# Kernel optimization log

Measured on AMD Instinct MI355X. Metric: run time of the kernel, lower is better.

Reference implementation:

```python
import jax, jax.numpy as jnp
import numpy as np

B = 1_048_576
NUM_USERS = 6041
NUM_MOVIES = 3953
EMB_DIM = 32
NUM_GENRES = 18
HIDDEN = [64, 32, 16]
WIDE_DIM = NUM_USERS + NUM_MOVIES + 3 + NUM_GENRES  # gender, age, occupation scalars
DEEP_IN = 2 * EMB_DIM + 3 + NUM_GENRES              # = 85


def setup_inputs() -> dict:
    key = jax.random.key(0)
    ks = jax.random.split(key, 20)
    inp = {
        "user_ids": jax.random.randint(ks[0], (B,), 0, NUM_USERS),
        "movie_ids": jax.random.randint(ks[1], (B,), 0, NUM_MOVIES),
        "gender": jax.random.uniform(ks[2], (B,), dtype=jnp.float32),
        "age": jax.random.uniform(ks[3], (B,), dtype=jnp.float32),
        "occupation": jax.random.uniform(ks[4], (B,), dtype=jnp.float32),
        "genres": jax.random.uniform(ks[5], (B, NUM_GENRES), dtype=jnp.float32),
        # wide linear (out_features=1): weight vector + scalar bias
        "wide_W": jax.random.normal(ks[6], (WIDE_DIM,), dtype=jnp.float32) * 0.01,
        "wide_b": jnp.zeros((), dtype=jnp.float32),
        # embedding tables
        "user_table": jax.random.normal(ks[7], (NUM_USERS, EMB_DIM), dtype=jnp.float32) * 0.05,
        "movie_table": jax.random.normal(ks[8], (NUM_MOVIES, EMB_DIM), dtype=jnp.float32) * 0.05,
        # deep MLP params (stored as [in, out])
        "W1": jax.random.normal(ks[9], (DEEP_IN, HIDDEN[0]), dtype=jnp.float32) * 0.05,
        "b1": jnp.zeros((HIDDEN[0],), dtype=jnp.float32),
        "W2": jax.random.normal(ks[10], (HIDDEN[0], HIDDEN[1]), dtype=jnp.float32) * 0.05,
        "b2": jnp.zeros((HIDDEN[1],), dtype=jnp.float32),
        "W3": jax.random.normal(ks[11], (HIDDEN[1], HIDDEN[2]), dtype=jnp.float32) * 0.05,
        "b3": jnp.zeros((HIDDEN[2],), dtype=jnp.float32),
        "W4": jax.random.normal(ks[12], (HIDDEN[2], 1), dtype=jnp.float32) * 0.05,
        "b4": jnp.zeros((1,), dtype=jnp.float32),
    }
    return inp


def reference(user_ids, movie_ids, gender, age, occupation, genres,
              wide_W, wide_b, user_table, movie_table,
              W1, b1, W2, b2, W3, b3, W4, b4):
    nu = user_table.shape[0]
    nm = movie_table.shape[0]
    # dense (non-one-hot) part of the wide input: [B, 3 + num_genres]
    rest = jnp.concatenate(
        [gender[:, None], age[:, None], occupation[:, None], genres], axis=1)
    # one_hot @ W  ==  gather of the corresponding weight entries (same math,
    # without materializing the [B, nu+nm+21] one-hot matrix)
    w_user = wide_W[:nu]
    w_movie = wide_W[nu:nu + nm]
    w_rest = wide_W[nu + nm:]
    wide_out = w_user[user_ids] + w_movie[movie_ids] + rest @ w_rest + wide_b  # [B]

    # deep path (dropout is identity at inference)
    u_emb = user_table[user_ids]    # [B, 32]
    m_emb = movie_table[movie_ids]  # [B, 32]
    h = jnp.concatenate([u_emb, m_emb, rest], axis=1)  # [B, 85]
    h = jax.nn.relu(h @ W1 + b1)
    h = jax.nn.relu(h @ W2 + b2)
    h = jax.nn.relu(h @ W3 + b3)
    deep_out = (h @ W4 + b4)[:, 0]  # [B]

    return jax.nn.sigmoid(wide_out + deep_out)  # [B]
```

## Files before the change

### kernel.cpp

```cpp
#include <hip/hip_runtime.h>

#define NUSERS  6041
#define NMOVIES 3953
#define EMB     32
#define NGEN    18
#define H1N     64
#define H2N     32
#define H3N     16

typedef __bf16 bf16_t;
typedef bf16_t bf16x8 __attribute__((ext_vector_type(8)));
typedef bf16_t bf16x4 __attribute__((ext_vector_type(4)));
typedef float  f32x4  __attribute__((ext_vector_type(4)));
typedef float  f32x8  __attribute__((ext_vector_type(8)));

__device__ __forceinline__ f32x4 mfma16(bf16x8 a, bf16x8 b, f32x4 c) {
    return __builtin_amdgcn_mfma_f32_16x16x32_bf16(a, b, c, 0, 0, 0);
}
__device__ __forceinline__ bf16x8 cvt8(f32x8 v) {
    bf16x8 o;
    #pragma unroll
    for (int i = 0; i < 8; ++i) o[i] = (bf16_t)v[i];
    return o;
}

#define L1STRIDE 68
#define L2STRIDE 36
#define RSTRIDE  28
#define RBUFSZ   (16 * RSTRIDE)

#define TAB_U4   (NUSERS * EMB / 4)
#define TAB_M4   (NMOVIES * EMB / 4)
#define TAB4TOT  (TAB_U4 + TAB_M4)
#define TABBLOCKS ((TAB4TOT + 255) / 256)

#define WPACK_HALF 9216
#define WPACK_BYTES 18432

__global__ __launch_bounds__(256)
void prep_pack(const float* __restrict__ user_table,
               const float* __restrict__ movie_table,
               const float* __restrict__ W1,
               const float* __restrict__ b1,
               const float* __restrict__ W2,
               const float* __restrict__ W3,
               const float* __restrict__ wide_W,
               bf16_t* __restrict__ utab,
               bf16_t* __restrict__ mtab,
               bf16_t* __restrict__ wpack)
{
    const int t = threadIdx.x;
    const int b = blockIdx.x;

    if (b < TABBLOCKS) {
        const int u = b * 256 + t;
        if (u < TAB4TOT) {
            if (u < TAB_U4) {
                float4 v = *(const float4*)(user_table + (size_t)u * 4);
                bf16x4 o; o[0]=(bf16_t)v.x; o[1]=(bf16_t)v.y; o[2]=(bf16_t)v.z; o[3]=(bf16_t)v.w;
                *(bf16x4*)(utab + (size_t)u * 4) = o;
            } else {
                const int w = u - TAB_U4;
                float4 v = *(const float4*)(movie_table + (size_t)w * 4);
                bf16x4 o; o[0]=(bf16_t)v.x; o[1]=(bf16_t)v.y; o[2]=(bf16_t)v.z; o[3]=(bf16_t)v.w;
                *(bf16x4*)(mtab + (size_t)w * 4) = o;
            }
        }
        return;
    }

    const int l  = t & 63;
    const int f0 = t >> 6;
    const int m  = l & 15;
    const int q  = l >> 4;
    const float* wr = wide_W + NUSERS + NMOVIES;

    #pragma unroll
    for (int p = 0; p < 5; ++p) {
        const int f = f0 + p * 4;
        if (f >= 18) break;
        bf16x8 frag;
        #pragma unroll
        for (int j = 0; j < 8; ++j) {
            float v = 0.0f;
            if (f < 12) {
                const int kt = f >> 2, nt = f & 3;
                if (kt < 2) {
                    v = W1[(kt * 32 + q * 8 + j) * H1N + nt * 16 + m];
                } else if (q < 3) {
                    if (j < 6)       v = W1[(67 + 6 * q + j) * H1N + nt * 16 + m];
                    else if (q == 0) v = W1[(64 + (j - 6)) * H1N + nt * 16 + m];
                    else if (q == 1) v = (j == 6) ? W1[66 * H1N + nt * 16 + m]
                                                 : b1[nt * 16 + m];
                }
            } else if (f == 12) {
                if (m == 0) {
                    if (q < 3 && j < 6)        v = wr[3 + 6 * q + j];
                    else if (q == 0)           v = wr[j - 6];
                    else if (q == 1 && j == 6) v = wr[2];
                    else if (q == 2 && j == 6) v = 1.0f;
                }
            } else if (f < 17) {
                const int kt = (f - 13) >> 1, nt = (f - 13) & 1;
                const int u = (2 * kt + (j >> 2)) * 16 + q * 4 + (j & 3);
                v = W2[u * H2N + nt * 16 + m];
            } else {
                const int u = (j >> 2) * 16 + q * 4 + (j & 3);
                v = W3[u * H3N + m];
            }
            frag[j] = (bf16_t)v;
        }
        *(bf16x8*)(wpack + ((size_t)f * 64 + l) * 8) = frag;
    }
}

__global__ __launch_bounds__(256, 2)
void wd_fwd_main2(const int*   __restrict__ user_ids,
                  const int*   __restrict__ movie_ids,
                  const float* __restrict__ gender,
                  const float* __restrict__ age,
                  const float* __restrict__ occupation,
                  const float* __restrict__ genres,
                  const float* __restrict__ wide_W,
                  const float* __restrict__ wide_b,
                  const float* __restrict__ b2,
                  const float* __restrict__ b3,
                  const float* __restrict__ W4,
                  const float* __restrict__ b4,
                  const bf16_t* __restrict__ utab,
                  const bf16_t* __restrict__ mtab,
                  const bf16_t* __restrict__ wpack,
                  float*       __restrict__ out,
                  int n)
{
    const int lane = threadIdx.x & 63;
    const int m    = lane & 15;
    const int quad = lane >> 4;

    const bf16x8* wp = (const bf16x8*)wpack;
    bf16x8 B1f[3][4];
    #pragma unroll
    for (int kt = 0; kt < 3; ++kt)
        #pragma unroll
        for (int nt = 0; nt < 4; ++nt)
            B1f[kt][nt] = wp[(kt * 4 + nt) * 64 + lane];
    const bf16x8 Bwf = wp[12 * 64 + lane];
    bf16x8 B2f[2][2];
    #pragma unroll
    for (int kt = 0; kt < 2; ++kt)
        #pragma unroll
        for (int nt = 0; nt < 2; ++nt)
            B2f[kt][nt] = wp[(13 + kt * 2 + nt) * 64 + lane];
    const bf16x8 B3f = wp[17 * 64 + lane];

    f32x4 bias2[2], bias3, w4f;
    bias2[0] = *(const f32x4*)(b2 + quad * 4);
    bias2[1] = *(const f32x4*)(b2 + 16 + quad * 4);
    bias3    = *(const f32x4*)(b3 + quad * 4);
    w4f      = *(const f32x4*)(W4 + quad * 4);
    const float b4v = b4[0];
    const float wb0 = wide_b[0];

    const int nst   = (n + 31) >> 5;
    const int gwave = (blockIdx.x * blockDim.x + threadIdx.x) >> 6;
    const int nw    = (gridDim.x * blockDim.x) >> 6;
    int niter = 0;
    if (gwave < nst) niter = (nst - gwave + nw - 1) / nw;
    if (niter == 0) return;

    int st_c = gwave;
    int st_n = st_c + nw; if (st_n >= nst) st_n = st_c;

#define GATHER(row_, uid_, mid_, A0_, A1_, A2_) {                              \
    A0_ = *(const bf16x8*)(utab + (size_t)(uid_) * EMB + quad * 8);            \
    A1_ = *(const bf16x8*)(mtab + (size_t)(mid_) * EMB + quad * 8);            \
    float2 g01 = {0.f,0.f}, g23 = {0.f,0.f}, g45 = {0.f,0.f};                  \
    float s6 = 0.f, s7 = 0.f;                                                  \
    if (quad < 3) {                                                            \
        const float* gp_ = genres + (size_t)(row_) * NGEN + quad * 6;          \
        g01 = *(const float2*)gp_;                                             \
        g23 = *(const float2*)(gp_ + 2);                                       \
        g45 = *(const float2*)(gp_ + 4);                                       \
    }                                                                          \
    if (quad == 0)      { s6 = gender[row_]; s7 = age[row_]; }                 \
    else if (quad == 1) { s6 = occupation[row_]; s7 = 1.0f; }                  \
    else if (quad == 2) { s6 = wide_W[uid_] + wide_W[NUSERS + (mid_)] + wb0; } \
    A2_[0] = (bf16_t)g01.x; A2_[1] = (bf16_t)g01.y;                            \
    A2_[2] = (bf16_t)g23.x; A2_[3] = (bf16_t)g23.y;                            \
    A2_[4] = (bf16_t)g45.x; A2_[5] = (bf16_t)g45.y;                            \
    A2_[6] = (bf16_t)s6;    A2_[7] = (bf16_t)s7; }

    int ra = st_c * 32 + m;      if (ra >= n) ra = n - 1;
    int rb = st_c * 32 + 16 + m; if (rb >= n) rb = n - 1;
    int uidA = user_ids[ra], midA = movie_ids[ra];
    int uidB = user_ids[rb], midB = movie_ids[rb];
    bf16x8 A0a, A1a, A2a, A0b, A1b, A2b;
    GATHER(ra, uidA, midA, A0a, A1a, A2a);
    GATHER(rb, uidB, midB, A0b, A1b, A2b);
    int ran = st_n * 32 + m;      if (ran >= n) ran = n - 1;
    int rbn = st_n * 32 + 16 + m; if (rbn >= n) rbn = n - 1;
    int uidAn = user_ids[ran], midAn = movie_ids[ran];
    int uidBn = user_ids[rbn], midBn = movie_ids[rbn];

    for (int i = 0; i < niter; ++i) {
        const bool more = (i + 1 < niter);
        bf16x8 A0an = A0a, A1an = A1a, A2an = A2a;
        bf16x8 A0bn = A0b, A1bn = A1b, A2bn = A2b;
        int uidA2 = uidAn, midA2 = midAn, uidB2 = uidBn, midB2 = midBn;
        int st_n2 = st_n;
        if (more) {
            int ran_ = st_n * 32 + m;      if (ran_ >= n) ran_ = n - 1;
            int rbn_ = st_n * 32 + 16 + m; if (rbn_ >= n) rbn_ = n - 1;
            GATHER(ran_, uidAn, midAn, A0an, A1an, A2an);
            GATHER(rbn_, uidBn, midBn, A0bn, A1bn, A2bn);
            st_n2 = st_n + nw; if (st_n2 >= nst) st_n2 = st_n;
            int ra2 = st_n2 * 32 + m;      if (ra2 >= n) ra2 = n - 1;
            int rb2 = st_n2 * 32 + 16 + m; if (rb2 >= n) rb2 = n - 1;
            uidA2 = user_ids[ra2]; midA2 = movie_ids[ra2];
            uidB2 = user_ids[rb2]; midB2 = movie_ids[rb2];
        }

        const f32x4 z4 = {0.f, 0.f, 0.f, 0.f};
        f32x4 accwA = mfma16(Bwf, A2a, z4);
        f32x4 accwB = mfma16(Bwf, A2b, z4);

        f32x4 aA[4], aB[4];
        #pragma unroll
        for (int nt = 0; nt < 4; ++nt) {
            aA[nt] = mfma16(B1f[2][nt], A2a, z4);
            aB[nt] = mfma16(B1f[2][nt], A2b, z4);
        }
        #pragma unroll
        for (int nt = 0; nt < 4; ++nt) {
            aA[nt] = mfma16(B1f[1][nt], A1a, aA[nt]);
            aB[nt] = mfma16(B1f[1][nt], A1b, aB[nt]);
        }
        #pragma unroll
        for (int nt = 0; nt < 4; ++nt) {
            aA[nt] = mfma16(B1f[0][nt], A0a, aA[nt]);
            aB[nt] = mfma16(B1f[0][nt], A0b, aB[nt]);
        }

        bf16x8 L2a[2], L2b[2];
        #pragma unroll
        for (int kt = 0; kt < 2; ++kt)
            #pragma unroll
            for (int r = 0; r < 4; ++r) {
                L2a[kt][r]     = (bf16_t)fmaxf(aA[2 * kt][r],     0.f);
                L2a[kt][4 + r] = (bf16_t)fmaxf(aA[2 * kt + 1][r], 0.f);
                L2b[kt][r]     = (bf16_t)fmaxf(aB[2 * kt][r],     0.f);
                L2b[kt][4 + r] = (bf16_t)fmaxf(aB[2 * kt + 1][r], 0.f);
            }

        f32x4 c2A[2], c2B[2];
        #pragma unroll
        for (int nt = 0; nt < 2; ++nt) {
            c2A[nt] = mfma16(B2f[1][nt], L2a[1], mfma16(B2f[0][nt], L2a[0], bias2[nt]));
            c2B[nt] = mfma16(B2f[1][nt], L2b[1], mfma16(B2f[0][nt], L2b[0], bias2[nt]));
        }

        bf16x8 L3a, L3b;
        #pragma unroll
        for (int r = 0; r < 4; ++r) {
            L3a[r]     = (bf16_t)fmaxf(c2A[0][r], 0.f);
            L3a[4 + r] = (bf16_t)fmaxf(c2A[1][r], 0.f);
            L3b[r]     = (bf16_t)fmaxf(c2B[0][r], 0.f);
            L3b[4 + r] = (bf16_t)fmaxf(c2B[1][r], 0.f);
        }

        f32x4 c3A = mfma16(B3f, L3a, bias3);
        f32x4 c3B = mfma16(B3f, L3b, bias3);

        float pA = fmaxf(c3A[0], 0.f) * w4f[0] + fmaxf(c3A[1], 0.f) * w4f[1]
                 + fmaxf(c3A[2], 0.f) * w4f[2] + fmaxf(c3A[3], 0.f) * w4f[3];
        float pB = fmaxf(c3B[0], 0.f) * w4f[0] + fmaxf(c3B[1], 0.f) * w4f[1]
                 + fmaxf(c3B[2], 0.f) * w4f[2] + fmaxf(c3B[3], 0.f) * w4f[3];
        pA += __shfl_xor(pA, 16, 64);  pA += __shfl_xor(pA, 32, 64);
        pB += __shfl_xor(pB, 16, 64);  pB += __shfl_xor(pB, 32, 64);

        if (lane < 16) {
            const int base = st_c << 5;
            const int oa = base + lane, ob = base + 16 + lane;
            const float zA = pA + accwA[0] + b4v;
            const float zB = pB + accwB[0] + b4v;
            if (oa < n) out[oa] = 1.0f / (1.0f + __expf(-zA));
            if (ob < n) out[ob] = 1.0f / (1.0f + __expf(-zB));
        }

        if (more) {
            A0a = A0an; A1a = A1an; A2a = A2an;
            A0b = A0bn; A1b = A1bn; A2b = A2bn;
            uidAn = uidA2; midAn = midA2; uidBn = uidB2; midBn = midB2;
            st_c = st_n; st_n = st_n2;
        }
    }
#undef GATHER
}

struct Pref {
    float4 u0, u1, m0, m1;
    float  wu, wm;
};

__global__ __launch_bounds__(256)
void wd_fwd_pipe(const int*   __restrict__ user_ids,
                 const int*   __restrict__ movie_ids,
                 const float* __restrict__ gender,
                 const float* __restrict__ age,
                 const float* __restrict__ occupation,
                 const float* __restrict__ genres,
                 const float* __restrict__ wide_W,
                 const float* __restrict__ wide_b,
                 const float* __restrict__ user_table,
                 const float* __restrict__ movie_table,
                 const float* __restrict__ W1,
                 const float* __restrict__ b1,
                 const float* __restrict__ W2,
                 const float* __restrict__ b2,
                 const float* __restrict__ W3,
                 const float* __restrict__ b3,
                 const float* __restrict__ W4,
                 const float* __restrict__ b4,
                 float*       __restrict__ out,
                 int n)
{
    const int lane = threadIdx.x & 63;
    const int wib  = threadIdx.x >> 6;
    const int m    = lane & 15;
    const int quad = lane >> 4;

    __shared__ float lds_rest[4][2 * RBUFSZ];
    __shared__ float lds1[4][16 * L1STRIDE];
    __shared__ float lds2[4][16 * L2STRIDE];
    float* __restrict__ rbase = lds_rest[wib];
    float* __restrict__ L1p   = lds1[wib];
    float* __restrict__ L2p   = lds2[wib];

    for (int k = lane; k < 2 * RBUFSZ; k += 64) rbase[k] = 0.0f;

    bf16x8 B1f[3][4];
    #pragma unroll
    for (int kt = 0; kt < 3; ++kt)
        #pragma unroll
        for (int nt = 0; nt < 4; ++nt) {
            bf16x8 f;
            #pragma unroll
            for (int j = 0; j < 8; ++j) {
                const int k  = kt * 32 + quad * 8 + j;
                const float v = (k < 85) ? W1[k * H1N + nt * 16 + m] : 0.0f;
                f[j] = (bf16_t)v;
            }
            B1f[kt][nt] = f;
        }
    bf16x8 Bwf;
    {
        const float* wr = wide_W + NUSERS + NMOVIES;
        #pragma unroll
        for (int j = 0; j < 8; ++j) {
            const int k = 64 + quad * 8 + j;
            float v = 0.0f;
            if (m == 0) { if (k < 85) v = wr[k - 64]; else if (k == 85) v = 1.0f; }
            Bwf[j] = (bf16_t)v;
        }
    }
    bf16x8 B2f[2][2];
    #pragma unroll
    for (int kt = 0; kt < 2; ++kt)
        #pragma unroll
        for (int nt = 0; nt < 2; ++nt) {
            bf16x8 f;
            #pragma unroll
            for (int j = 0; j < 8; ++j)
                f[j] = (bf16_t)W2[(kt * 32 + quad * 8 + j) * H2N + nt * 16 + m];
            B2f[kt][nt] = f;
        }
    bf16x8 B3f;
    #pragma unroll
    for (int j = 0; j < 8; ++j) B3f[j] = (bf16_t)W3[(quad * 8 + j) * H3N + m];

    float bias1[4], bias2[2];
    #pragma unroll
    for (int nt = 0; nt < 4; ++nt) bias1[nt] = b1[nt * 16 + m];
    #pragma unroll
    for (int nt = 0; nt < 2; ++nt) bias2[nt] = b2[nt * 16 + m];
    const float bias3 = b3[m];
    const float w4v   = W4[m];
    const float b4v   = b4[0];
    const float wb0   = wide_b[0];

    const int ntiles = (n + 15) >> 4;
    const int gwave  = blockIdx.x * 4 + wib;
    const int nwaves = gridDim.x * 4;
    int niter = 0;
    if (gwave < ntiles) niter = (ntiles - gwave + nwaves - 1) / nwaves;
    const long gmax = (long)n * NGEN - 1;

#define LOAD_IDS(tt, U, M) { int rr = (tt) * 16 + m; rr = rr < n ? rr : n - 1; \
                             U = user_ids[rr]; M = movie_ids[rr]; }
#define LOAD_GENRES(tt, G, SC) { \
    const long gb = (long)(tt) * (16 * NGEN); \
    _Pragma("unroll") \
    for (int r = 0; r < 4; ++r) { long idx = gb + lane + r * 64; \
        idx = idx < gmax ? idx : gmax; G[r] = genres[idx]; } \
    { long idx = gb + lane + 256; idx = idx < gmax ? idx : gmax; \
      G[4] = (lane < 32) ? genres[idx] : 0.0f; } \
    { int rr = (tt) * 16 + m; rr = rr < n ? rr : n - 1; \
      const float* sp = (quad == 0) ? gender : (quad == 1) ? age : occupation; \
      SC = (quad < 3) ? sp[rr] : 0.0f; } }
#define WRITE_RBUF(B, G, SC) { \
    float* rb_ = rbase + (B) * RBUFSZ; \
    _Pragma("unroll") \
    for (int r = 0; r < 4; ++r) { int gi = lane + r * 64; int rw = gi / NGEN; \
        int cl = gi - rw * NGEN; rb_[rw * RSTRIDE + 3 + cl] = G[r]; } \
    if (lane < 32) { int gi = lane + 256; int rw = gi / NGEN; int cl = gi - rw * NGEN; \
        rb_[rw * RSTRIDE + 3 + cl] = G[4]; } \
    if (quad < 3) rb_[m * RSTRIDE + quad] = SC; }
#define ISSUE_GATHER(UID, MID, P) { \
    const float4* up_ = (const float4*)(user_table + (size_t)(UID) * EMB + quad * 8); \
    P.u0 = up_[0]; P.u1 = up_[1]; \
    const float4* mp_ = (const float4*)(movie_table + (size_t)(MID) * EMB + quad * 8); \
    P.m0 = mp_[0]; P.m1 = mp_[1]; \
    P.wu = wide_W[UID]; P.wm = wide_W[NUSERS + (MID)]; }

    if (niter > 0) {
        int t_c = gwave;
        int t_n = t_c + nwaves; if (t_n >= ntiles) t_n = t_c;

        int uid_c, mid_c, uid_n, mid_n, uid_n2, mid_n2;
        float gg_c[5], sc_c, gg_n[5], sc_n;
        Pref P_c, P_n;

        LOAD_IDS(t_c, uid_c, mid_c);
        LOAD_GENRES(t_c, gg_c, sc_c);
        ISSUE_GATHER(uid_c, mid_c, P_c);
        LOAD_IDS(t_n, uid_n, mid_n);
        WRITE_RBUF(0, gg_c, sc_c);
        uid_n2 = uid_n; mid_n2 = mid_n;
        int buf = 0;

        for (int i = 0; i < niter; ++i) {
            const float* rb = rbase + buf * RBUFSZ;
            const float4* sA = (const float4*)(rb + m * RSTRIDE + quad * 8);
            float4 a2a = sA[0], a2b = sA[1];

            const bool more = (i + 1 < niter);
            int t_n2 = t_n;
            if (more) {
                LOAD_GENRES(t_n, gg_n, sc_n);
                ISSUE_GATHER(uid_n, mid_n, P_n);
                t_n2 = t_n + nwaves; if (t_n2 >= ntiles) t_n2 = t_n;
                LOAD_IDS(t_n2, uid_n2, mid_n2);
            }

            const int base = t_c << 4;
            f32x8 vf;
            vf[0]=P_c.u0.x; vf[1]=P_c.u0.y; vf[2]=P_c.u0.z; vf[3]=P_c.u0.w;
            vf[4]=P_c.u1.x; vf[5]=P_c.u1.y; vf[6]=P_c.u1.z; vf[7]=P_c.u1.w;
            bf16x8 A0 = cvt8(vf);
            vf[0]=P_c.m0.x; vf[1]=P_c.m0.y; vf[2]=P_c.m0.z; vf[3]=P_c.m0.w;
            vf[4]=P_c.m1.x; vf[5]=P_c.m1.y; vf[6]=P_c.m1.z; vf[7]=P_c.m1.w;
            bf16x8 A1 = cvt8(vf);
            vf[0]=a2a.x; vf[1]=a2a.y; vf[2]=a2a.z; vf[3]=a2a.w;
            vf[4]=a2b.x; vf[5]=a2b.y; vf[6]=a2b.z; vf[7]=a2b.w;
            if (quad == 2) vf[5] = P_c.wu + P_c.wm + wb0;
            bf16x8 A2 = cvt8(vf);

            f32x4 accw = mfma16(A2, Bwf, (f32x4){0.f, 0.f, 0.f, 0.f});

            f32x4 acc[4];
            #pragma unroll
            for (int nt = 0; nt < 4; ++nt) {
                f32x4 c = {bias1[nt], bias1[nt], bias1[nt], bias1[nt]};
                c = mfma16(A0, B1f[0][nt], c);
                c = mfma16(A1, B1f[1][nt], c);
                c = mfma16(A2, B1f[2][nt], c);
                acc[nt] = c;
            }
            #pragma unroll
            for (int nt = 0; nt < 4; ++nt)
                #pragma unroll
                for (int r = 0; r < 4; ++r)
                    L1p[(quad * 4 + r) * L1STRIDE + nt * 16 + m] = fmaxf(acc[nt][r], 0.0f);

            bf16x8 AL2[2];
            #pragma unroll
            for (int kt = 0; kt < 2; ++kt) {
                const float4* s = (const float4*)(L1p + m * L1STRIDE + kt * 32 + quad * 8);
                float4 a = s[0], b = s[1];
                f32x8 t8; t8[0]=a.x; t8[1]=a.y; t8[2]=a.z; t8[3]=a.w;
                t8[4]=b.x; t8[5]=b.y; t8[6]=b.z; t8[7]=b.w;
                AL2[kt] = cvt8(t8);
            }

            f32x4 acc2[2];
            #pragma unroll
            for (int nt = 0; nt < 2; ++nt) {
                f32x4 c = {bias2[nt], bias2[nt], bias2[nt], bias2[nt]};
                c = mfma16(AL2[0], B2f[0][nt], c);
                c = mfma16(AL2[1], B2f[1][nt], c);
                acc2[nt] = c;
            }
            #pragma unroll
            for (int nt = 0; nt < 2; ++nt)
                #pragma unroll
                for (int r = 0; r < 4; ++r)
                    L2p[(quad * 4 + r) * L2STRIDE + nt * 16 + m] = fmaxf(acc2[nt][r], 0.0f);

            bf16x8 AL3;
            {
                const float4* s = (const float4*)(L2p + m * L2STRIDE + quad * 8);
                float4 a = s[0], b = s[1];
                f32x8 t8; t8[0]=a.x; t8[1]=a.y; t8[2]=a.z; t8[3]=a.w;
                t8[4]=b.x; t8[5]=b.y; t8[6]=b.z; t8[7]=b.w;
                AL3 = cvt8(t8);
            }

            f32x4 acc3 = mfma16(AL3, B3f, (f32x4){bias3, bias3, bias3, bias3});

            float t0 = fmaxf(acc3[0], 0.0f) * w4v + accw[0];
            float t1 = fmaxf(acc3[1], 0.0f) * w4v + accw[1];
            float t2 = fmaxf(acc3[2], 0.0f) * w4v + accw[2];
            float t3 = fmaxf(acc3[3], 0.0f) * w4v + accw[3];
            #pragma unroll
            for (int off = 1; off < 16; off <<= 1) {
                t0 += __shfl_xor(t0, off, 64);
                t1 += __shfl_xor(t1, off, 64);
                t2 += __shfl_xor(t2, off, 64);
                t3 += __shfl_xor(t3, off, 64);
            }
            if (m < 4) {
                float zv = t0;
                zv = (m == 1) ? t1 : zv;
                zv = (m == 2) ? t2 : zv;
                zv = (m == 3) ? t3 : zv;
                zv += b4v;
                const int orow = base + quad * 4 + m;
                if (orow < n) out[orow] = 1.0f / (1.0f + __expf(-zv));
            }

            if (more) {
                WRITE_RBUF(buf ^ 1, gg_n, sc_n);
                P_c = P_n;
                uid_c = uid_n; mid_c = mid_n;
                uid_n = uid_n2; mid_n = mid_n2;
                t_c = t_n; t_n = t_n2;
                buf ^= 1;
            }
        }
    }
#undef LOAD_IDS
#undef LOAD_GENRES
#undef WRITE_RBUF
#undef ISSUE_GATHER
}

extern "C" void kernel_launch(void* const* d_in, const int* in_sizes, int n_in,
                              void* d_out, int out_size, void* d_ws, size_t ws_size,
                              hipStream_t stream)
{
    const int*   user_ids   = (const int*)  d_in[0];
    const int*   movie_ids  = (const int*)  d_in[1];
    const float* gender     = (const float*)d_in[2];
    const float* age        = (const float*)d_in[3];
    const float* occupation = (const float*)d_in[4];
    const float* genres     = (const float*)d_in[5];
    const float* wide_W     = (const float*)d_in[6];
    const float* wide_b     = (const float*)d_in[7];
    const float* user_table = (const float*)d_in[8];
    const float* movie_table= (const float*)d_in[9];
    const float* W1         = (const float*)d_in[10];
    const float* b1         = (const float*)d_in[11];
    const float* W2         = (const float*)d_in[12];
    const float* b2         = (const float*)d_in[13];
    const float* W3         = (const float*)d_in[14];
    const float* b3         = (const float*)d_in[15];
    const float* W4         = (const float*)d_in[16];
    const float* b4         = (const float*)d_in[17];
    float*       out        = (float*)d_out;

    const int n = in_sizes[0];

    const size_t utab_bytes = ((size_t)NUSERS  * EMB * 2 + 255) & ~(size_t)255;
    const size_t mtab_bytes = ((size_t)NMOVIES * EMB * 2 + 255) & ~(size_t)255;
    const size_t need = utab_bytes + mtab_bytes + WPACK_BYTES;

    if (d_ws != nullptr && ws_size >= need) {
        bf16_t* utab  = (bf16_t*)d_ws;
        bf16_t* mtab  = (bf16_t*)((char*)d_ws + utab_bytes);
        bf16_t* wpack = (bf16_t*)((char*)d_ws + utab_bytes + mtab_bytes);

        prep_pack<<<TABBLOCKS + 1, 256, 0, stream>>>(user_table, movie_table,
                                                     W1, b1, W2, W3, wide_W,
                                                     utab, mtab, wpack);
        wd_fwd_main2<<<2048, 256, 0, stream>>>(user_ids, movie_ids,
                                               gender, age, occupation, genres,
                                               wide_W, wide_b, b2, b3, W4, b4,
                                               utab, mtab, wpack, out, n);
    } else {
        wd_fwd_pipe<<<1024, 256, 0, stream>>>(user_ids, movie_ids, gender, age, occupation,
                                              genres, wide_W, wide_b, user_table, movie_table,
                                              W1, b1, W2, b2, W3, b3, W4, b4, out, n);
    }
}
```

Before: 227.3 us.

## Pre-pack genres into padded bf16 rows and restructure main loop to 16-row tiles

Adds a prep pass that stages each block's genres through shared memory and writes them as 24-wide bf16 rows to workspace, so the main kernel reads one aligned 16-byte vector per quad instead of strided float2 loads. The main kernel switches from 32-row to 16-row tiles with a two-stage ping-pong gather/compute pipeline, halves the grid to 1024 blocks, and remaps the W1/wide weight packing to the new column order. The cost is an extra full pass over genres (read fp32, write bf16) plus a rest buffer that scales with the batch, and the workspace fallback triggers if the buffer does not fit.

```diff
diff --git a/kernel.cpp b/kernel.cpp
--- a/kernel.cpp
+++ b/kernel.cpp
@@ -34,26 +34,75 @@
 #define TAB4TOT  (TAB_U4 + TAB_M4)
 #define TABBLOCKS ((TAB4TOT + 255) / 256)
 
-#define WPACK_HALF 9216
+#define RESTW 24
+
 #define WPACK_BYTES 18432
 
 __global__ __launch_bounds__(256)
-void prep_pack(const float* __restrict__ user_table,
+void prep_all2(const float* __restrict__ genres,
+               const float* __restrict__ user_table,
                const float* __restrict__ movie_table,
                const float* __restrict__ W1,
                const float* __restrict__ b1,
                const float* __restrict__ W2,
                const float* __restrict__ W3,
                const float* __restrict__ wide_W,
+               bf16_t* __restrict__ rest,
                bf16_t* __restrict__ utab,
                bf16_t* __restrict__ mtab,
-               bf16_t* __restrict__ wpack)
+               bf16_t* __restrict__ wpack,
+               int n)
 {
-    const int t = threadIdx.x;
-    const int b = blockIdx.x;
-
-    if (b < TABBLOCKS) {
-        const int u = b * 256 + t;
+    const int t  = threadIdx.x;
+    const int b  = blockIdx.x;
+    const int gB = (n + 255) >> 8;
+
+    if (b < gB) {
+        const int r0 = b * 256;
+        __shared__ float gbuf[256 * NGEN];
+        if ((n & 1) == 0) {
+            const float4* gsrc = (const float4*)genres;
+            const int totF4  = (n * NGEN) >> 2;
+            const int f4base = (r0 >> 1) * 9;
+            #pragma unroll
+            for (int s = 0; s < 5; ++s) {
+                const int gi = t + s * 256;
+                if (gi < 1152) {
+                    int idx = f4base + gi;
+                    if (idx > totF4 - 1) idx = totF4 - 1;
+                    *(float4*)(gbuf + gi * 4) = gsrc[idx];
+                }
+            }
+        } else {
+            for (int gi = t; gi < 256 * NGEN; gi += 256) {
+                long idx = (long)r0 * NGEN + gi;
+                long mx  = (long)n * NGEN - 1;
+                if (idx > mx) idx = mx;
+                gbuf[gi] = genres[idx];
+            }
+        }
+        __syncthreads();
+        const int r = r0 + t;
+        if (r < n) {
+            float x[NGEN];
+            #pragma unroll
+            for (int c = 0; c < NGEN; ++c) x[c] = gbuf[t * NGEN + c];
+            bf16x8 c0, c1, c2;
+            #pragma unroll
+            for (int j = 0; j < 8; ++j) { c0[j] = (bf16_t)x[j]; c1[j] = (bf16_t)x[8 + j]; }
+            c2[0] = (bf16_t)x[16]; c2[1] = (bf16_t)x[17];
+            #pragma unroll
+            for (int j = 2; j < 8; ++j) c2[j] = (bf16_t)0.0f;
+            bf16_t* op = rest + (size_t)r * RESTW;
+            *(bf16x8*)(op)      = c0;
+            *(bf16x8*)(op + 8)  = c1;
+            *(bf16x8*)(op + 16) = c2;
+        }
+        return;
+    }
+
+    if (b < gB + TABBLOCKS) {
+        const int u = (b - gB) * 256 + t;
         if (u < TAB4TOT) {
             if (u < TAB_U4) {
                 float4 v = *(const float4*)(user_table + (size_t)u * 4);
@@ -87,18 +136,32 @@
                 const int kt = f >> 2, nt = f & 3;
                 if (kt < 2) {
                     v = W1[(kt * 32 + q * 8 + j) * H1N + nt * 16 + m];
-                } else if (q < 3) {
-                    if (j < 6)       v = W1[(67 + 6 * q + j) * H1N + nt * 16 + m];
-                    else if (q == 0) v = W1[(64 + (j - 6)) * H1N + nt * 16 + m];
-                    else if (q == 1) v = (j == 6) ? W1[66 * H1N + nt * 16 + m]
-                                                 : b1[nt * 16 + m];
+                } else {
+                    int row = -1;
+                    if (q == 0)      row = 67 + j;
+                    else if (q == 1) row = 75 + j;
+                    else if (q == 2) {
+                        if (j == 0) row = 83;
+                        else if (j == 1) row = 84;
+                        else if (j == 2) row = 64;
+                        else if (j == 3) row = 65;
+                        else if (j == 4) row = 66;
+                        else if (j == 5) v = b1[nt * 16 + m];
+                    }
+                    if (row >= 0) v = W1[row * H1N + nt * 16 + m];
                 }
             } else if (f == 12) {
                 if (m == 0) {
-                    if (q < 3 && j < 6)        v = wr[3 + 6 * q + j];
-                    else if (q == 0)           v = wr[j - 6];
-                    else if (q == 1 && j == 6) v = wr[2];
-                    else if (q == 2 && j == 6) v = 1.0f;
+                    if (q == 0)      v = wr[3 + j];
+                    else if (q == 1) v = wr[11 + j];
+                    else if (q == 2) {
+                        if (j == 0) v = wr[19];
+                        else if (j == 1) v = wr[20];
+                        else if (j == 2) v = wr[0];
+                        else if (j == 3) v = wr[1];
+                        else if (j == 4) v = wr[2];
+                        else if (j == 6) v = 1.0f;
+                    }
                 }
             } else if (f < 17) {
                 const int kt = (f - 13) >> 1, nt = (f - 13) & 1;
@@ -115,12 +178,11 @@
 }
 
 __global__ __launch_bounds__(256, 2)
-void wd_fwd_main2(const int*   __restrict__ user_ids,
+void wd_fwd_main3(const int*   __restrict__ user_ids,
                   const int*   __restrict__ movie_ids,
                   const float* __restrict__ gender,
                   const float* __restrict__ age,
                   const float* __restrict__ occupation,
-                  const float* __restrict__ genres,
                   const float* __restrict__ wide_W,
                   const float* __restrict__ wide_b,
                   const float* __restrict__ b2,
@@ -129,6 +191,7 @@
                   const float* __restrict__ b4,
                   const bf16_t* __restrict__ utab,
                   const bf16_t* __restrict__ mtab,
+                  const bf16_t* __restrict__ rest,
                   const bf16_t* __restrict__ wpack,
                   float*       __restrict__ out,
                   int n)
@@ -161,140 +224,104 @@
     const float b4v = b4[0];
     const float wb0 = wide_b[0];
 
-    const int nst   = (n + 31) >> 5;
+    const int nst   = (n + 15) >> 4;
     const int gwave = (blockIdx.x * blockDim.x + threadIdx.x) >> 6;
     const int nw    = (gridDim.x * blockDim.x) >> 6;
     int niter = 0;
     if (gwave < nst) niter = (nst - gwave + nw - 1) / nw;
     if (niter == 0) return;
 
-    int st_c = gwave;
-    int st_n = st_c + nw; if (st_n >= nst) st_n = st_c;
-
 #define GATHER(row_, uid_, mid_, A0_, A1_, A2_) {                              \
     A0_ = *(const bf16x8*)(utab + (size_t)(uid_) * EMB + quad * 8);            \
     A1_ = *(const bf16x8*)(mtab + (size_t)(mid_) * EMB + quad * 8);            \
-    float2 g01 = {0.f,0.f}, g23 = {0.f,0.f}, g45 = {0.f,0.f};                  \
-    float s6 = 0.f, s7 = 0.f;                                                  \
-    if (quad < 3) {                                                            \
-        const float* gp_ = genres + (size_t)(row_) * NGEN + quad * 6;          \
-        g01 = *(const float2*)gp_;                                             \
-        g23 = *(const float2*)(gp_ + 2);                                       \
-        g45 = *(const float2*)(gp_ + 4);                                       \
+    bf16x8 t_;                                                                 \
+    _Pragma("unroll")                                                          \
+    for (int j_ = 0; j_ < 8; ++j_) t_[j_] = (bf16_t)0.0f;                      \
+    if (quad < 3) t_ = *(const bf16x8*)(rest + (size_t)(row_) * RESTW + quad * 8); \
+    if (quad == 2) {                                                           \
+        const float g_ = gender[row_], a_ = age[row_], o_ = occupation[row_];  \
+        const float w_ = wide_W[uid_] + wide_W[NUSERS + (mid_)] + wb0;         \
+        t_[2] = (bf16_t)g_; t_[3] = (bf16_t)a_; t_[4] = (bf16_t)o_;            \
+        t_[5] = (bf16_t)1.0f; t_[6] = (bf16_t)w_; t_[7] = (bf16_t)0.0f;        \
     }                                                                          \
-    if (quad == 0)      { s6 = gender[row_]; s7 = age[row_]; }                 \
-    else if (quad == 1) { s6 = occupation[row_]; s7 = 1.0f; }                  \
-    else if (quad == 2) { s6 = wide_W[uid_] + wide_W[NUSERS + (mid_)] + wb0; } \
-    A2_[0] = (bf16_t)g01.x; A2_[1] = (bf16_t)g01.y;                            \
-    A2_[2] = (bf16_t)g23.x; A2_[3] = (bf16_t)g23.y;                            \
-    A2_[4] = (bf16_t)g45.x; A2_[5] = (bf16_t)g45.y;                            \
-    A2_[6] = (bf16_t)s6;    A2_[7] = (bf16_t)s7; }
-
-    int ra = st_c * 32 + m;      if (ra >= n) ra = n - 1;
-    int rb = st_c * 32 + 16 + m; if (rb >= n) rb = n - 1;
-    int uidA = user_ids[ra], midA = movie_ids[ra];
-    int uidB = user_ids[rb], midB = movie_ids[rb];
-    bf16x8 A0a, A1a, A2a, A0b, A1b, A2b;
-    GATHER(ra, uidA, midA, A0a, A1a, A2a);
-    GATHER(rb, uidB, midB, A0b, A1b, A2b);
-    int ran = st_n * 32 + m;      if (ran >= n) ran = n - 1;
-    int rbn = st_n * 32 + 16 + m; if (rbn >= n) rbn = n - 1;
-    int uidAn = user_ids[ran], midAn = movie_ids[ran];
-    int uidBn = user_ids[rbn], midBn = movie_ids[rbn];
-
-    for (int i = 0; i < niter; ++i) {
-        const bool more = (i + 1 < niter);
-        bf16x8 A0an = A0a, A1an = A1a, A2an = A2a;
-        bf16x8 A0bn = A0b, A1bn = A1b, A2bn = A2b;
-        int uidA2 = uidAn, midA2 = midAn, uidB2 = uidBn, midB2 = midBn;
-        int st_n2 = st_n;
-        if (more) {
-            int ran_ = st_n * 32 + m;      if (ran_ >= n) ran_ = n - 1;
-            int rbn_ = st_n * 32 + 16 + m; if (rbn_ >= n) rbn_ = n - 1;
-            GATHER(ran_, uidAn, midAn, A0an, A1an, A2an);
-            GATHER(rbn_, uidBn, midBn, A0bn, A1bn, A2bn);
-            st_n2 = st_n + nw; if (st_n2 >= nst) st_n2 = st_n;
-            int ra2 = st_n2 * 32 + m;      if (ra2 >= n) ra2 = n - 1;
-            int rb2 = st_n2 * 32 + 16 + m; if (rb2 >= n) rb2 = n - 1;
-            uidA2 = user_ids[ra2]; midA2 = movie_ids[ra2];
-            uidB2 = user_ids[rb2]; midB2 = movie_ids[rb2];
-        }
-
-        const f32x4 z4 = {0.f, 0.f, 0.f, 0.f};
-        f32x4 accwA = mfma16(Bwf, A2a, z4);
-        f32x4 accwB = mfma16(Bwf, A2b, z4);
-
-        f32x4 aA[4], aB[4];
-        #pragma unroll
-        for (int nt = 0; nt < 4; ++nt) {
-            aA[nt] = mfma16(B1f[2][nt], A2a, z4);
-            aB[nt] = mfma16(B1f[2][nt], A2b, z4);
-        }
-        #pragma unroll
-        for (int nt = 0; nt < 4; ++nt) {
-            aA[nt] = mfma16(B1f[1][nt], A1a, aA[nt]);
-            aB[nt] = mfma16(B1f[1][nt], A1b, aB[nt]);
-        }
-        #pragma unroll
-        for (int nt = 0; nt < 4; ++nt) {
-            aA[nt] = mfma16(B1f[0][nt], A0a, aA[nt]);
-            aB[nt] = mfma16(B1f[0][nt], A0b, aB[nt]);
-        }
-
-        bf16x8 L2a[2], L2b[2];
-        #pragma unroll
-        for (int kt = 0; kt < 2; ++kt)
-            #pragma unroll
-            for (int r = 0; r < 4; ++r) {
-                L2a[kt][r]     = (bf16_t)fmaxf(aA[2 * kt][r],     0.f);
-                L2a[kt][4 + r] = (bf16_t)fmaxf(aA[2 * kt + 1][r], 0.f);
-                L2b[kt][r]     = (bf16_t)fmaxf(aB[2 * kt][r],     0.f);
-                L2b[kt][4 + r] = (bf16_t)fmaxf(aB[2 * kt + 1][r], 0.f);
-            }
-
-        f32x4 c2A[2], c2B[2];
-        #pragma unroll
-        for (int nt = 0; nt < 2; ++nt) {
-            c2A[nt] = mfma16(B2f[1][nt], L2a[1], mfma16(B2f[0][nt], L2a[0], bias2[nt]));
-            c2B[nt] = mfma16(B2f[1][nt], L2b[1], mfma16(B2f[0][nt], L2b[0], bias2[nt]));
-        }
-
-        bf16x8 L3a, L3b;
-        #pragma unroll
-        for (int r = 0; r < 4; ++r) {
-            L3a[r]     = (bf16_t)fmaxf(c2A[0][r], 0.f);
-            L3a[4 + r] = (bf16_t)fmaxf(c2A[1][r], 0.f);
-            L3b[r]     = (bf16_t)fmaxf(c2B[0][r], 0.f);
-            L3b[4 + r] = (bf16_t)fmaxf(c2B[1][r], 0.f);
-        }
-
-        f32x4 c3A = mfma16(B3f, L3a, bias3);
-        f32x4 c3B = mfma16(B3f, L3b, bias3);
-
-        float pA = fmaxf(c3A[0], 0.f) * w4f[0] + fmaxf(c3A[1], 0.f) * w4f[1]
-                 + fmaxf(c3A[2], 0.f) * w4f[2] + fmaxf(c3A[3], 0.f) * w4f[3];
-        float pB = fmaxf(c3B[0], 0.f) * w4f[0] + fmaxf(c3B[1], 0.f) * w4f[1]
-                 + fmaxf(c3B[2], 0.f) * w4f[2] + fmaxf(c3B[3], 0.f) * w4f[3];
-        pA += __shfl_xor(pA, 16, 64);  pA += __shfl_xor(pA, 32, 64);
-        pB += __shfl_xor(pB, 16, 64);  pB += __shfl_xor(pB, 32, 64);
-
-        if (lane < 16) {
-            const int base = st_c << 5;
-            const int oa = base + lane, ob = base + 16 + lane;
-            const float zA = pA + accwA[0] + b4v;
-            const float zB = pB + accwB[0] + b4v;
-            if (oa < n) out[oa] = 1.0f / (1.0f + __expf(-zA));
-            if (ob < n) out[ob] = 1.0f / (1.0f + __expf(-zB));
-        }
-
-        if (more) {
-            A0a = A0an; A1a = A1an; A2a = A2an;
-            A0b = A0bn; A1b = A1bn; A2b = A2bn;
-            uidAn = uidA2; midAn = midA2; uidBn = uidB2; midBn = midB2;
-            st_c = st_n; st_n = st_n2;
-        }
+    A2_ = t_; }
+
+#define COMPUTE(A0_, A1_, A2_, tile_) {                                        \
+    f32x4 accw_ = mfma16(Bwf, A2_, (f32x4){0.f, 0.f, 0.f, 0.f});               \
+    f32x4 acc_[4];                                                             \
+    _Pragma("unroll")                                                          \
+    for (int nt = 0; nt < 4; ++nt) {                                           \
+        f32x4 c_ = {0.f, 0.f, 0.f, 0.f};                                       \
+        c_ = mfma16(B1f[2][nt], A2_, c_);                                      \
+        c_ = mfma16(B1f[1][nt], A1_, c_);                                      \
+        c_ = mfma16(B1f[0][nt], A0_, c_);                                      \
+        acc_[nt] = c_;                                                         \
+    }                                                                          \
+    bf16x8 L2_[2];                                                             \
+    _Pragma("unroll")                                                          \
+    for (int kt = 0; kt < 2; ++kt)                                             \
+        _Pragma("unroll")                                                      \
+        for (int r_ = 0; r_ < 4; ++r_) {                                       \
+            L2_[kt][r_]     = (bf16_t)fmaxf(acc_[2 * kt][r_],     0.f);        \
+            L2_[kt][4 + r_] = (bf16_t)fmaxf(acc_[2 * kt + 1][r_], 0.f);        \
+        }                                                                      \
+    f32x4 c2_[2];                                                              \
+    _Pragma("unroll")                                                          \
+    for (int nt = 0; nt < 2; ++nt)                                             \
+        c2_[nt] = mfma16(B2f[1][nt], L2_[1],                                   \
+                         mfma16(B2f[0][nt], L2_[0], bias2[nt]));               \
+    bf16x8 L3_;                                                                \
+    _Pragma("unroll")                                                          \
+    for (int r_ = 0; r_ < 4; ++r_) {                                           \
+        L3_[r_]     = (bf16_t)fmaxf(c2_[0][r_], 0.f);                          \
+        L3_[4 + r_] = (bf16_t)fmaxf(c2_[1][r_], 0.f);                          \
+    }                                                                          \
+    f32x4 c3_ = mfma16(B3f, L3_, bias3);                                       \
+    float p_ = fmaxf(c3_[0], 0.f) * w4f[0] + fmaxf(c3_[1], 0.f) * w4f[1]       \
+             + fmaxf(c3_[2], 0.f) * w4f[2] + fmaxf(c3_[3], 0.f) * w4f[3];      \
+    p_ += __shfl_xor(p_, 16, 64);                                              \
+    p_ += __shfl_xor(p_, 32, 64);                                              \
+    if (lane < 16) {                                                           \
+        const int orow_ = ((tile_) << 4) + lane;                               \
+        if (orow_ < n) {                                                       \
+            const float zv_ = p_ + accw_[0] + b4v;                             \
+            out[orow_] = 1.0f / (1.0f + __expf(-zv_));                         \
+        }                                                                      \
+    } }
+
+    int tc = gwave;
+    int rc = tc * 16 + m; if (rc >= n) rc = n - 1;
+    int uid0 = user_ids[rc], mid0 = movie_ids[rc];
+    bf16x8 P0a, P0b, P0c;
+    GATHER(rc, uid0, mid0, P0a, P0b, P0c);
+
+    int tp = tc + nw; if (tp >= nst) tp = nst - 1;
+    int rp = tp * 16 + m; if (rp >= n) rp = n - 1;
+    int uidp = user_ids[rp], midp = movie_ids[rp];
+
+    int done = 0;
+    while (done + 1 < niter) {
+        int tq = tp + nw; if (tq >= nst) tq = nst - 1;
+        int rq = tq * 16 + m; if (rq >= n) rq = n - 1;
+        int uidq = user_ids[rq], midq = movie_ids[rq];
+        bf16x8 P1a, P1b, P1c;
+        GATHER(rp, uidp, midp, P1a, P1b, P1c);
+        COMPUTE(P0a, P0b, P0c, tc);
+
+        int tr = tq + nw; if (tr >= nst) tr = nst - 1;
+        int rr = tr * 16 + m; if (rr >= n) rr = n - 1;
+        GATHER(rq, uidq, midq, P0a, P0b, P0c);
+        int uidr = user_ids[rr], midr = movie_ids[rr];
+        COMPUTE(P1a, P1b, P1c, tp);
+
+        tc = tq; tp = tr; rp = rr;
+        uidp = uidr; midp = midr;
+        done += 2;
     }
+    if (done < niter) COMPUTE(P0a, P0b, P0c, tc);
+
 #undef GATHER
+#undef COMPUTE
 }
 
 struct Pref {
@@ -580,22 +607,27 @@
 
     const int n = in_sizes[0];
 
-    const size_t utab_bytes = ((size_t)NUSERS  * EMB * 2 + 255) & ~(size_t)255;
-    const size_t mtab_bytes = ((size_t)NMOVIES * EMB * 2 + 255) & ~(size_t)255;
-    const size_t need = utab_bytes + mtab_bytes + WPACK_BYTES;
+    const size_t utab_bytes  = ((size_t)NUSERS  * EMB * 2 + 255) & ~(size_t)255;
+    const size_t mtab_bytes  = ((size_t)NMOVIES * EMB * 2 + 255) & ~(size_t)255;
+    const size_t wpack_bytes = (WPACK_BYTES + 255) & ~(size_t)255;
+    const size_t rest_bytes  = (size_t)n * RESTW * 2;
+    const size_t need = utab_bytes + mtab_bytes + wpack_bytes + rest_bytes;
 
     if (d_ws != nullptr && ws_size >= need) {
         bf16_t* utab  = (bf16_t*)d_ws;
         bf16_t* mtab  = (bf16_t*)((char*)d_ws + utab_bytes);
         bf16_t* wpack = (bf16_t*)((char*)d_ws + utab_bytes + mtab_bytes);
-
-        prep_pack<<<TABBLOCKS + 1, 256, 0, stream>>>(user_table, movie_table,
-                                                     W1, b1, W2, W3, wide_W,
-                                                     utab, mtab, wpack);
-        wd_fwd_main2<<<2048, 256, 0, stream>>>(user_ids, movie_ids,
-                                               gender, age, occupation, genres,
+        bf16_t* rest  = (bf16_t*)((char*)d_ws + utab_bytes + mtab_bytes + wpack_bytes);
+
+        const int gB = (n + 255) >> 8;
+        prep_all2<<<gB + TABBLOCKS + 1, 256, 0, stream>>>(genres,
+                                                          user_table, movie_table,
+                                                          W1, b1, W2, W3, wide_W,
+                                                          rest, utab, mtab, wpack, n);
+        wd_fwd_main3<<<1024, 256, 0, stream>>>(user_ids, movie_ids,
+                                               gender, age, occupation,
                                                wide_W, wide_b, b2, b3, W4, b4,
-                                               utab, mtab, wpack, out, n);
+                                               utab, mtab, rest, wpack, out, n);
     } else {
         wd_fwd_pipe<<<1024, 256, 0, stream>>>(user_ids, movie_ids, gender, age, occupation,
                                               genres, wide_W, wide_b, user_table, movie_table,
```

New measurement: 236.7 us. 4.2% more time.
